# Kernel optimization log

Hardware: AMD Instinct MI355X
Metric: run time of the kernel (lower is better)

Reference implementation:

```python
import jax, jax.numpy as jnp
import numpy as np

N = 100_000   # nodes
E = 3_200_000 # edges
D = 128       # input feature dim


def setup_inputs() -> dict:
    key = jax.random.key(0)
    ks = jax.random.split(key, 6)
    x = jax.random.normal(ks[0], (N, D), dtype=jnp.float32)
    edge_index = jax.random.randint(ks[1], (2, E), 0, N, dtype=jnp.int32)
    # Glorot-ish init for the three GCN layer weights
    W1 = jax.random.normal(ks[2], (D, 32), dtype=jnp.float32) * (1.0 / np.sqrt(D))
    W2 = jax.random.normal(ks[3], (32, 16), dtype=jnp.float32) * (1.0 / np.sqrt(32))
    W3 = jax.random.normal(ks[4], (16, 1), dtype=jnp.float32) * (1.0 / np.sqrt(16))
    b1 = jnp.zeros((32,), jnp.float32)
    b2 = jnp.zeros((16,), jnp.float32)
    b3 = jnp.zeros((1,), jnp.float32)
    return {"x": x, "edge_index": edge_index, "W1": W1, "b1": b1,
            "W2": W2, "b2": b2, "W3": W3, "b3": b3}


def _gcn_edges(edge_index, num_nodes):
    # PyG GCNConv default: add self-loops, symmetric normalization
    loop = jnp.arange(num_nodes, dtype=edge_index.dtype)
    src = jnp.concatenate([edge_index[0], loop])
    dst = jnp.concatenate([edge_index[1], loop])
    deg = jax.ops.segment_sum(jnp.ones_like(dst, jnp.float32), dst, num_segments=num_nodes)
    dis = jax.lax.rsqrt(deg)  # deg >= 1 because of self-loops
    norm = dis[src] * dis[dst]  # [E+N]
    return src, dst, norm


def _gcn_layer(h, W, b, src, dst, norm, num_nodes):
    # linear transform, then normalized gather -> scatter-add aggregation
    hw = h @ W                                  # [N, out]
    msg = norm[:, None] * hw[src]               # [E+N, out]
    out = jax.ops.segment_sum(msg, dst, num_segments=num_nodes)
    return out + b


def reference(x, edge_index, W1, b1, W2, b2, W3, b3):
    src, dst, norm = _gcn_edges(edge_index, N)
    h = jax.nn.relu(_gcn_layer(x, W1, b1, src, dst, norm, N))
    h = jax.nn.relu(_gcn_layer(h, W2, b2, src, dst, norm, N))
    return _gcn_layer(h, W3, b3, src, dst, norm, N)  # [N, 1]
```

## Files before the change

### kernel.cpp

```cpp
#include <hip/hip_runtime.h>
#include <hip/hip_fp16.h>

#define NN 100000
#define NE 3200000
#define DI 128

#define RSH 7
#define RMASK 127
#define NB ((NN + RMASK) >> RSH)
#define CAP 5120
#define SB 512
#define SCHUNK ((NE + SB - 1) / SB)
#define MAXE ((SCHUNK + 1023) / 1024)
#define SK ((CAP + 1023) / 1024)

#define OFF_GCUR   ((size_t)100000)
#define OFF_ROWPTR ((size_t)100800)
#define OFF_DEG    ((size_t)200800)
#define OFF_REC    ((size_t)300800)
#define OFF_HWD1   (OFF_REC + (size_t)NB * CAP)
#define OFF_HWD2   (OFF_HWD1 + (size_t)16 * NN)
#define OFF_HWD3   (OFF_HWD2 + (size_t)8 * NN)

#define ACC8(r) { const __half2* hp_ = reinterpret_cast<const __half2*>(&(r));      \
    float2 f0_ = __half22float2(hp_[0]), f1_ = __half22float2(hp_[1]);              \
    float2 f2_ = __half22float2(hp_[2]), f3_ = __half22float2(hp_[3]);              \
    a0 += f0_.x; a1 += f0_.y; a2 += f1_.x; a3 += f1_.y;                             \
    a4 += f2_.x; a5 += f2_.y; a6 += f3_.x; a7 += f3_.y; }

__global__ __launch_bounds__(1024) void scatter_kernel(const int* __restrict__ src,
                                                       const int* __restrict__ dst,
                                                       int* __restrict__ gcur,
                                                       unsigned* __restrict__ rec) {
    __shared__ int lh[NB];
    __shared__ int lbase[NB];
    int tid = threadIdx.x;
    for (int i = tid; i < NB; i += 1024) lh[i] = 0;
    __syncthreads();
    int base = blockIdx.x * SCHUNK;
    int end = min(base + SCHUNK, NE);
    int keys[MAXE], rank[MAXE];
#pragma unroll
    for (int i = 0; i < MAXE; i++) {
        int e = base + tid + i * 1024;
        bool ok = e < end;
        keys[i] = ok ? dst[e] : 0;
        rank[i] = ok ? atomicAdd(&lh[keys[i] >> RSH], 1) : 0;
    }
    __syncthreads();
    for (int i = tid; i < NB; i += 1024) {
        int c = lh[i];
        lbase[i] = c ? atomicAdd(&gcur[i], c) : 0;
    }
    __syncthreads();
#pragma unroll
    for (int i = 0; i < MAXE; i++) {
        int e = base + tid + i * 1024;
        if (e < end) {
            int d = keys[i];
            int b = d >> RSH;
            int pos = lbase[b] + rank[i];
            if (pos < CAP)
                rec[(size_t)b * CAP + pos] = ((unsigned)src[e] << RSH) | (unsigned)(d & RMASK);
        }
    }
}

__global__ __launch_bounds__(1024) void sort_kernel(const int* __restrict__ gcur,
                                                    unsigned* __restrict__ rec,
                                                    int* __restrict__ rowptr,
                                                    int* __restrict__ deg,
                                                    float* __restrict__ dis) {
    __shared__ int cnt[128];
    __shared__ int sc[128];
    int tid = threadIdx.x, b = blockIdx.x;
    if (tid < 128) cnt[tid] = 0;
    __syncthreads();
    int count = min(gcur[b], CAP);
    size_t rbeg = (size_t)b * CAP;
    unsigned myrec[SK];
    int myrank[SK];
#pragma unroll
    for (int k = 0; k < SK; k++) {
        int j = tid + k * 1024;
        if (j < count) {
            unsigned r = rec[rbeg + j];
            myrec[k] = r;
            myrank[k] = atomicAdd(&cnt[r & RMASK], 1);
        } else {
            myrec[k] = 0; myrank[k] = 0;
        }
    }
    __syncthreads();
    if (tid < 128) sc[tid] = cnt[tid];
    __syncthreads();
    for (int d = 1; d < 128; d <<= 1) {
        int v = (tid < 128 && tid >= d) ? sc[tid - d] : 0;
        __syncthreads();
        if (tid < 128) sc[tid] += v;
        __syncthreads();
    }
    if (tid < 128) {
        int excl = sc[tid] - cnt[tid];
        int node = (b << RSH) + tid;
        if (node < NN) {
            rowptr[node] = (int)rbeg + excl;
            deg[node] = cnt[tid];
            dis[node] = rsqrtf((float)cnt[tid] + 1.0f);
        }
        cnt[tid] = excl;
    }
    __syncthreads();
#pragma unroll
    for (int k = 0; k < SK; k++) {
        int j = tid + k * 1024;
        if (j < count) {
            unsigned r = myrec[k];
            int pos = cnt[r & RMASK] + myrank[k];
            rec[rbeg + pos] = r >> RSH;
        }
    }
}

__global__ __launch_bounds__(256) void gemm1_kernel(const float* __restrict__ x,
                                                    const float* __restrict__ W,
                                                    const float* __restrict__ dis,
                                                    __half* __restrict__ out) {
    __shared__ float Ws[DI][32];
    __shared__ float xs[32][DI + 4];
    int tid = threadIdx.x;
    for (int i4 = tid; i4 < DI * 32 / 4; i4 += 256) {
        float4 w = reinterpret_cast<const float4*>(W)[i4];
        int base = i4 * 4;
        *reinterpret_cast<float4*>(&Ws[base / 32][base % 32]) = w;
    }
    int node0 = blockIdx.x * 32;
    for (int i4 = tid; i4 < 32 * DI / 4; i4 += 256) {
        int base = i4 * 4;
        int nl = base / DI, k = base % DI;
        int node = node0 + nl;
        float4 v = (node < NN) ? reinterpret_cast<const float4*>(x)[((size_t)node * DI + k) / 4]
                               : make_float4(0.f, 0.f, 0.f, 0.f);
        *reinterpret_cast<float4*>(&xs[nl][k]) = v;
    }
    __syncthreads();
    int nl = tid >> 3;
    int c4 = (tid & 7) * 4;
    int node = node0 + nl;
    if (node >= NN) return;
    float a0 = 0.f, a1 = 0.f, a2 = 0.f, a3 = 0.f;
#pragma unroll 8
    for (int k4 = 0; k4 < DI; k4 += 4) {
        float4 xv = *reinterpret_cast<const float4*>(&xs[nl][k4]);
        float4 w0 = *reinterpret_cast<const float4*>(&Ws[k4 + 0][c4]);
        float4 w1 = *reinterpret_cast<const float4*>(&Ws[k4 + 1][c4]);
        float4 w2 = *reinterpret_cast<const float4*>(&Ws[k4 + 2][c4]);
        float4 w3 = *reinterpret_cast<const float4*>(&Ws[k4 + 3][c4]);
        a0 += xv.x * w0.x + xv.y * w1.x + xv.z * w2.x + xv.w * w3.x;
        a1 += xv.x * w0.y + xv.y * w1.y + xv.z * w2.y + xv.w * w3.y;
        a2 += xv.x * w0.z + xv.y * w1.z + xv.z * w2.z + xv.w * w3.z;
        a3 += xv.x * w0.w + xv.y * w1.w + xv.z * w2.w + xv.w * w3.w;
    }
    float dn = dis[node];
    __half2 h0 = __floats2half2_rn(dn * a0, dn * a1);
    __half2 h1 = __floats2half2_rn(dn * a2, dn * a3);
    __half2* op = reinterpret_cast<__half2*>(out + (size_t)node * 32 + c4);
    op[0] = h0;
    op[1] = h1;
}

__global__ __launch_bounds__(256) void agg32_fused_kernel(const int* __restrict__ rowptr,
                                                          const int* __restrict__ deg,
                                                          const int* __restrict__ srcs,
                                                          const __half* __restrict__ hwd1,
                                                          const float* __restrict__ dis,
                                                          const float* __restrict__ b1,
                                                          const float* __restrict__ W2,
                                                          __half2* __restrict__ hwd2) {
    __shared__ float hc[64][33];
    __shared__ float W2s[32][16];
    int tid = threadIdx.x;
    for (int i = tid; i < 512; i += 256) W2s[i >> 4][i & 15] = W2[i];
    int gtid = blockIdx.x * 256 + tid;
    int node = gtid >> 2;
    int lane = tid & 3;
    int nl = tid >> 2;
    int c8 = lane * 8;
    if (node < NN) {
        int beg = rowptr[node];
        int end = beg + deg[node];
        const float4* hv = reinterpret_cast<const float4*>(hwd1);
        float a0, a1, a2, a3, a4, a5, a6, a7;
        {
            float4 sr = hv[(size_t)node * 4 + lane];
            const __half2* hp = reinterpret_cast<const __half2*>(&sr);
            float2 f0 = __half22float2(hp[0]), f1 = __half22float2(hp[1]);
            float2 f2 = __half22float2(hp[2]), f3 = __half22float2(hp[3]);
            a0 = f0.x; a1 = f0.y; a2 = f1.x; a3 = f1.y;
            a4 = f2.x; a5 = f2.y; a6 = f3.x; a7 = f3.y;
        }
        int j = beg;
        for (; j + 8 <= end; j += 8) {
            int i0 = srcs[j],     i1 = srcs[j + 1], i2 = srcs[j + 2], i3 = srcs[j + 3];
            int i4 = srcs[j + 4], i5 = srcs[j + 5], i6 = srcs[j + 6], i7 = srcs[j + 7];
            float4 r0 = hv[(size_t)i0 * 4 + lane];
            float4 r1 = hv[(size_t)i1 * 4 + lane];
            float4 r2 = hv[(size_t)i2 * 4 + lane];
            float4 r3 = hv[(size_t)i3 * 4 + lane];
            float4 r4 = hv[(size_t)i4 * 4 + lane];
            float4 r5 = hv[(size_t)i5 * 4 + lane];
            float4 r6 = hv[(size_t)i6 * 4 + lane];
            float4 r7 = hv[(size_t)i7 * 4 + lane];
            ACC8(r0); ACC8(r1); ACC8(r2); ACC8(r3);
            ACC8(r4); ACC8(r5); ACC8(r6); ACC8(r7);
        }
        for (; j < end; j++) {
            float4 r = hv[(size_t)srcs[j] * 4 + lane];
            ACC8(r);
        }
        float dn = dis[node];
        hc[nl][c8 + 0] = fmaxf(dn * a0 + b1[c8 + 0], 0.f);
        hc[nl][c8 + 1] = fmaxf(dn * a1 + b1[c8 + 1], 0.f);
        hc[nl][c8 + 2] = fmaxf(dn * a2 + b1[c8 + 2], 0.f);
        hc[nl][c8 + 3] = fmaxf(dn * a3 + b1[c8 + 3], 0.f);
        hc[nl][c8 + 4] = fmaxf(dn * a4 + b1[c8 + 4], 0.f);
        hc[nl][c8 + 5] = fmaxf(dn * a5 + b1[c8 + 5], 0.f);
        hc[nl][c8 + 6] = fmaxf(dn * a6 + b1[c8 + 6], 0.f);
        hc[nl][c8 + 7] = fmaxf(dn * a7 + b1[c8 + 7], 0.f);
    }
    __syncthreads();
    int node0 = blockIdx.x * 64;
    for (int o = tid; o < 64 * 8; o += 256) {
        int l = o >> 3, cp = o & 7;
        int n2 = node0 + l;
        if (n2 < NN) {
            float s0 = 0.f, s1 = 0.f;
#pragma unroll
            for (int k = 0; k < 32; k++) {
                float h = hc[l][k];
                s0 += h * W2s[k][2 * cp];
                s1 += h * W2s[k][2 * cp + 1];
            }
            float d2 = dis[n2];
            hwd2[(size_t)n2 * 8 + cp] = __floats2half2_rn(d2 * s0, d2 * s1);
        }
    }
}

__global__ __launch_bounds__(256) void agg16_fused_kernel(const int* __restrict__ rowptr,
                                                          const int* __restrict__ deg,
                                                          const int* __restrict__ srcs,
                                                          const __half* __restrict__ hwd2,
                                                          const float* __restrict__ dis,
                                                          const float* __restrict__ b2,
                                                          const float* __restrict__ W3,
                                                          __half* __restrict__ hwd3) {
    __shared__ float hc[128][17];
    __shared__ float W3s[16];
    int tid = threadIdx.x;
    if (tid < 16) W3s[tid] = W3[tid];
    int gtid = blockIdx.x * 256 + tid;
    int node = gtid >> 1;
    int lane = tid & 1;
    int nl = tid >> 1;
    int c8 = lane * 8;
    if (node < NN) {
        int beg = rowptr[node];
        int end = beg + deg[node];
        const float4* hv = reinterpret_cast<const float4*>(hwd2);
        float a0, a1, a2, a3, a4, a5, a6, a7;
        {
            float4 sr = hv[(size_t)node * 2 + lane];
            const __half2* hp = reinterpret_cast<const __half2*>(&sr);
            float2 f0 = __half22float2(hp[0]), f1 = __half22float2(hp[1]);
            float2 f2 = __half22float2(hp[2]), f3 = __half22float2(hp[3]);
            a0 = f0.x; a1 = f0.y; a2 = f1.x; a3 = f1.y;
            a4 = f2.x; a5 = f2.y; a6 = f3.x; a7 = f3.y;
        }
        int j = beg;
        for (; j + 8 <= end; j += 8) {
            int i0 = srcs[j],     i1 = srcs[j + 1], i2 = srcs[j + 2], i3 = srcs[j + 3];
            int i4 = srcs[j + 4], i5 = srcs[j + 5], i6 = srcs[j + 6], i7 = srcs[j + 7];
            float4 r0 = hv[(size_t)i0 * 2 + lane];
            float4 r1 = hv[(size_t)i1 * 2 + lane];
            float4 r2 = hv[(size_t)i2 * 2 + lane];
            float4 r3 = hv[(size_t)i3 * 2 + lane];
            float4 r4 = hv[(size_t)i4 * 2 + lane];
            float4 r5 = hv[(size_t)i5 * 2 + lane];
            float4 r6 = hv[(size_t)i6 * 2 + lane];
            float4 r7 = hv[(size_t)i7 * 2 + lane];
            ACC8(r0); ACC8(r1); ACC8(r2); ACC8(r3);
            ACC8(r4); ACC8(r5); ACC8(r6); ACC8(r7);
        }
        for (; j < end; j++) {
            float4 r = hv[(size_t)srcs[j] * 2 + lane];
            ACC8(r);
        }
        float dn = dis[node];
        hc[nl][c8 + 0] = fmaxf(dn * a0 + b2[c8 + 0], 0.f);
        hc[nl][c8 + 1] = fmaxf(dn * a1 + b2[c8 + 1], 0.f);
        hc[nl][c8 + 2] = fmaxf(dn * a2 + b2[c8 + 2], 0.f);
        hc[nl][c8 + 3] = fmaxf(dn * a3 + b2[c8 + 3], 0.f);
        hc[nl][c8 + 4] = fmaxf(dn * a4 + b2[c8 + 4], 0.f);
        hc[nl][c8 + 5] = fmaxf(dn * a5 + b2[c8 + 5], 0.f);
        hc[nl][c8 + 6] = fmaxf(dn * a6 + b2[c8 + 6], 0.f);
        hc[nl][c8 + 7] = fmaxf(dn * a7 + b2[c8 + 7], 0.f);
    }
    __syncthreads();
    int node0 = blockIdx.x * 128;
    if (tid < 128) {
        int n2 = node0 + tid;
        if (n2 < NN) {
            float s = 0.f;
#pragma unroll
            for (int k = 0; k < 16; k++) s += hc[tid][k] * W3s[k];
            hwd3[n2] = __float2half(dis[n2] * s);
        }
    }
}

__global__ __launch_bounds__(256) void agg1_kernel(const int* __restrict__ rowptr,
                                                   const int* __restrict__ deg,
                                                   const int* __restrict__ srcs,
                                                   const __half* __restrict__ hwd3,
                                                   const float* __restrict__ dis,
                                                   const float* __restrict__ b3,
                                                   float* __restrict__ out) {
    int node = blockIdx.x * 256 + threadIdx.x;
    if (node >= NN) return;
    int beg = rowptr[node];
    int end = beg + deg[node];
    float acc = __half2float(hwd3[node]);
    int j = beg;
    for (; j + 4 <= end; j += 4) {
        float v0 = __half2float(hwd3[srcs[j]]);
        float v1 = __half2float(hwd3[srcs[j + 1]]);
        float v2 = __half2float(hwd3[srcs[j + 2]]);
        float v3 = __half2float(hwd3[srcs[j + 3]]);
        acc += (v0 + v1) + (v2 + v3);
    }
    for (; j < end; j++) acc += __half2float(hwd3[srcs[j]]);
    out[node] = dis[node] * acc + b3[0];
}

extern "C" void kernel_launch(void* const* d_in, const int* in_sizes, int n_in,
                              void* d_out, int out_size, void* d_ws, size_t ws_size,
                              hipStream_t stream) {
    const float* x  = (const float*)d_in[0];
    const int*   ei = (const int*)d_in[1];
    const int*   src = ei;
    const int*   dst = ei + NE;
    const float* W1 = (const float*)d_in[2];
    const float* b1 = (const float*)d_in[3];
    const float* W2 = (const float*)d_in[4];
    const float* b2 = (const float*)d_in[5];
    const float* W3 = (const float*)d_in[6];
    const float* b3 = (const float*)d_in[7];
    float* out = (float*)d_out;
    float* ws  = (float*)d_ws;

    float*    dis    = ws;
    int*      gcur   = (int*)(ws + OFF_GCUR);
    int*      rowptr = (int*)(ws + OFF_ROWPTR);
    int*      deg    = (int*)(ws + OFF_DEG);
    unsigned* rec    = (unsigned*)(ws + OFF_REC);
    __half*   hwd1   = (__half*)(ws + OFF_HWD1);
    __half*   hwd2   = (__half*)(ws + OFF_HWD2);
    __half*   hwd3   = (__half*)(ws + OFF_HWD3);

    hipMemsetAsync(gcur, 0, NB * sizeof(int), stream);
    scatter_kernel<<<SB, 1024, 0, stream>>>(src, dst, gcur, rec);
    sort_kernel<<<NB, 1024, 0, stream>>>(gcur, rec, rowptr, deg, dis);
    gemm1_kernel<<<(NN + 31) / 32, 256, 0, stream>>>(x, W1, dis, hwd1);
    agg32_fused_kernel<<<((size_t)NN * 4 + 255) / 256, 256, 0, stream>>>(
        rowptr, deg, (const int*)rec, hwd1, dis, b1, W2, (__half2*)hwd2);
    agg16_fused_kernel<<<((size_t)NN * 2 + 255) / 256, 256, 0, stream>>>(
        rowptr, deg, (const int*)rec, hwd2, dis, b2, W3, hwd3);
    agg1_kernel<<<(NN + 255) / 256, 256, 0, stream>>>(rowptr, deg, (const int*)rec, hwd3, dis, b3, out);
}
```

Before: 186.3 us.

## Stage scatter records in shared memory for coalesced bucket writes, widen buckets

The scatter kernel now sorts each block's edge records by bucket in shared memory, using a block-wide prefix scan over bucket counts. It then writes them to global memory in contiguous runs per bucket instead of scattering each record directly. Buckets are widened to 256 nodes with a larger capacity, and there are half as many scatter blocks, each holding a larger chunk. The aim is more coalesced global writes, paid for with heavy shared memory use (about 62 KB per block), an extra scan with many barriers, and lower parallelism in the scatter step.

```diff
diff --git a/kernel.cpp b/kernel.cpp
--- a/kernel.cpp
+++ b/kernel.cpp
@@ -5,11 +5,11 @@
 #define NE 3200000
 #define DI 128
 
-#define RSH 7
-#define RMASK 127
+#define RSH 8
+#define RMASK 255
 #define NB ((NN + RMASK) >> RSH)
-#define CAP 5120
-#define SB 512
+#define CAP 9472
+#define SB 256
 #define SCHUNK ((NE + SB - 1) / SB)
 #define MAXE ((SCHUNK + 1023) / 1024)
 #define SK ((CAP + 1023) / 1024)
@@ -32,13 +32,17 @@
                                                        const int* __restrict__ dst,
                                                        int* __restrict__ gcur,
                                                        unsigned* __restrict__ rec) {
+    __shared__ unsigned lrec[SCHUNK];
+    __shared__ unsigned short lbkt[SCHUNK];
     __shared__ int lh[NB];
+    __shared__ int lofs[NB];
     __shared__ int lbase[NB];
     int tid = threadIdx.x;
     for (int i = tid; i < NB; i += 1024) lh[i] = 0;
     __syncthreads();
     int base = blockIdx.x * SCHUNK;
     int end = min(base + SCHUNK, NE);
+    int cnt_total = end - base;
     int keys[MAXE], rank[MAXE];
 #pragma unroll
     for (int i = 0; i < MAXE; i++) {
@@ -48,9 +52,19 @@
         rank[i] = ok ? atomicAdd(&lh[keys[i] >> RSH], 1) : 0;
     }
     __syncthreads();
-    for (int i = tid; i < NB; i += 1024) {
-        int c = lh[i];
-        lbase[i] = c ? atomicAdd(&gcur[i], c) : 0;
+    int* stmp = (int*)lrec;
+    int v = (tid < NB) ? lh[tid] : 0;
+    stmp[tid] = v;
+    __syncthreads();
+    for (int d = 1; d < 1024; d <<= 1) {
+        int t = (tid >= d) ? stmp[tid - d] : 0;
+        __syncthreads();
+        stmp[tid] += t;
+        __syncthreads();
+    }
+    if (tid < NB) {
+        lofs[tid] = stmp[tid] - v;
+        lbase[tid] = v ? atomicAdd(&gcur[tid], v) : 0;
     }
     __syncthreads();
 #pragma unroll
@@ -59,10 +73,17 @@
         if (e < end) {
             int d = keys[i];
             int b = d >> RSH;
-            int pos = lbase[b] + rank[i];
-            if (pos < CAP)
-                rec[(size_t)b * CAP + pos] = ((unsigned)src[e] << RSH) | (unsigned)(d & RMASK);
-        }
+            int slot = lofs[b] + rank[i];
+            lrec[slot] = ((unsigned)src[e] << RSH) | (unsigned)(d & RMASK);
+            lbkt[slot] = (unsigned short)b;
+        }
+    }
+    __syncthreads();
+    for (int j = tid; j < cnt_total; j += 1024) {
+        int b = lbkt[j];
+        int pos = lbase[b] + (j - lofs[b]);
+        if (pos < CAP)
+            rec[(size_t)b * CAP + pos] = lrec[j];
     }
 }
 
@@ -71,10 +92,10 @@
                                                     int* __restrict__ rowptr,
                                                     int* __restrict__ deg,
                                                     float* __restrict__ dis) {
-    __shared__ int cnt[128];
-    __shared__ int sc[128];
+    __shared__ int cnt[256];
+    __shared__ int sc[256];
     int tid = threadIdx.x, b = blockIdx.x;
-    if (tid < 128) cnt[tid] = 0;
+    if (tid < 256) cnt[tid] = 0;
     __syncthreads();
     int count = min(gcur[b], CAP);
     size_t rbeg = (size_t)b * CAP;
@@ -92,15 +113,15 @@
         }
     }
     __syncthreads();
-    if (tid < 128) sc[tid] = cnt[tid];
-    __syncthreads();
-    for (int d = 1; d < 128; d <<= 1) {
-        int v = (tid < 128 && tid >= d) ? sc[tid - d] : 0;
+    if (tid < 256) sc[tid] = cnt[tid];
+    __syncthreads();
+    for (int d = 1; d < 256; d <<= 1) {
+        int v = (tid < 256 && tid >= d) ? sc[tid - d] : 0;
         __syncthreads();
-        if (tid < 128) sc[tid] += v;
+        if (tid < 256) sc[tid] += v;
         __syncthreads();
     }
-    if (tid < 128) {
+    if (tid < 256) {
         int excl = sc[tid] - cnt[tid];
         int node = (b << RSH) + tid;
         if (node < NN) {
```

New measurement: 172.4 us. -7.5%, faster.
